# Kernel tuning notes

Measured on AMD Instinct MI355X. Metric: run time of the kernel, lower is better.

The kernel has to match this reference:

```python
import jax, jax.numpy as jnp
import numpy as np

S, B, F, H, L = 256, 64, 512, 512, 4
INV_SQRT_H = float(1.0 / np.sqrt(H))


def _ln(x, g, b, eps=1e-5):
    # torch nn.LayerNorm: biased variance, eps=1e-5
    mu = jnp.mean(x, axis=-1, keepdims=True)
    var = jnp.var(x, axis=-1, keepdims=True)
    return (x - mu) * jax.lax.rsqrt(var + eps) * g + b


def setup_inputs() -> dict:
    key = jax.random.key(0)
    k1, k2 = jax.random.split(key)
    x = jax.random.normal(k1, (S, B, F), dtype=jnp.float32)  # time-major [S,B,F]
    W = jax.random.normal(k2, (L, 6, F, H), dtype=jnp.float32) * 0.02  # q,k,v,i,f,o
    b = jnp.zeros((L, 6, H), jnp.float32)
    ln_g = jnp.ones((L, 6, H), jnp.float32)
    ln_b = jnp.zeros((L, 6, H), jnp.float32)
    return {"x": x, "W": W, "b": b, "ln_g": ln_g, "ln_b": ln_b}


def reference(x, W, b, ln_g, ln_b):
    # Dropout is identity (eval mode / p effectively 0).
    def step(carry, x_t):
        h, c, n = carry  # each [L,B,H]
        layer_input = x_t  # [B,F]
        hs, cs, ns = [], [], []
        for l in range(L):
            # all 6 gate projections in one einsum: [6,B,H]
            z = jnp.einsum('bf,gfh->gbh', layer_input, W[l]) + b[l][:, None, :]
            z = z.at[1].multiply(INV_SQRT_H)  # k = Wk(x)/sqrt(H) before LN
            z = _ln(z, ln_g[l][:, None, :], ln_b[l][:, None, :])
            q, k, v = z[0], z[1], z[2]
            i = jax.nn.sigmoid(z[3])
            f = jax.nn.sigmoid(z[4])
            o = jax.nn.sigmoid(z[5])
            # (k[:,:,None] @ v[:,None,:]).sum(dim=1) == k.sum(-1,keepdims)*v
            kv_sum = jnp.sum(k, axis=-1, keepdims=True) * v
            c_l = f * c[l] + i * kv_sum
            n_l = f * n[l] + i * k
            n_hat = n_l / (jnp.linalg.norm(n_l, axis=-1, keepdims=True) + 1e-8)
            h_l = o * jnp.tanh(q * n_hat)
            if l > 0:  # residual_conn
                h_l = h_l + layer_input
            layer_input = h_l
            hs.append(h_l); cs.append(c_l); ns.append(n_l)
        h = jnp.stack(hs); c = jnp.stack(cs); n = jnp.stack(ns)
        return (h, c, n), h[-1]

    init = tuple(jnp.zeros((L, B, H), x.dtype) for _ in range(3))
    (h, c, n), out = jax.lax.scan(step, init, x)  # out: [S,B,H] time-major
    return out, h, c, n
```

## Files before the change

kernel.cpp:

```cpp
#include <hip/hip_runtime.h>


typedef unsigned short u16;
typedef unsigned int   u32;
typedef short s8v  __attribute__((ext_vector_type(8)));
typedef float f16v __attribute__((ext_vector_type(16)));

#define S_    256
#define B_    64
#define F_    512
#define H_    512
#define L_    4
#define NG    3072
#define RALL  16384
#define CH    16
#define INV_SQRT_H 0.044194173824159216f

__device__ __forceinline__ float bu2f(u16 u) {
    union { u32 i; float f; } z; z.i = ((u32)u) << 16; return z.f;
}
__device__ __forceinline__ u16 f2bf(float f) {
    union { float f; u32 i; } z; z.f = f;
    u32 r = (z.i + 0x7FFFu + ((z.i >> 16) & 1u)) >> 16;
    return (u16)r;
}
__device__ __forceinline__ float sigm(float x)  { return 1.0f / (1.0f + __expf(-x)); }
__device__ __forceinline__ float tanhf_(float x){ return 2.0f / (1.0f + __expf(-2.0f * x)) - 1.0f; }
__device__ __forceinline__ float wred64(float v) {
    #pragma unroll
    for (int m = 1; m < 64; m <<= 1) v += __shfl_xor(v, m);
    return v;
}
__device__ __forceinline__ void gl_lds16(const u16* g, u16* l) {
    __builtin_amdgcn_global_load_lds((const __attribute__((address_space(1))) u32*)g,
                                     (__attribute__((address_space(3))) u32*)l, 16, 0, 0);
}
__device__ __forceinline__ void unp8(uint4 u, float* f) {
    f[0] = bu2f((u16)(u.x & 0xffff)); f[1] = bu2f((u16)(u.x >> 16));
    f[2] = bu2f((u16)(u.y & 0xffff)); f[3] = bu2f((u16)(u.y >> 16));
    f[4] = bu2f((u16)(u.z & 0xffff)); f[5] = bu2f((u16)(u.z >> 16));
    f[6] = bu2f((u16)(u.w & 0xffff)); f[7] = bu2f((u16)(u.w >> 16));
}
__device__ __forceinline__ uint4 pck8(const float* f) {
    uint4 u;
    u.x = (u32)f2bf(f[0]) | ((u32)f2bf(f[1]) << 16);
    u.y = (u32)f2bf(f[2]) | ((u32)f2bf(f[3]) << 16);
    u.z = (u32)f2bf(f[4]) | ((u32)f2bf(f[5]) << 16);
    u.w = (u32)f2bf(f[6]) | ((u32)f2bf(f[7]) << 16);
    return u;
}

__global__ void convw_k(const float* __restrict__ W, u16* __restrict__ WT) {
    __shared__ float tile[32][33];
    const int lg = blockIdx.z;
    const int h0 = blockIdx.x * 32, f0 = blockIdx.y * 32;
    const float* Wb = W  + (size_t)lg * F_ * H_;
    u16*        WTb = WT + (size_t)lg * F_ * H_;
    const int tx = threadIdx.x, ty = threadIdx.y;
    #pragma unroll
    for (int i = 0; i < 32; i += 8)
        tile[ty + i][tx] = Wb[(size_t)(f0 + ty + i) * H_ + h0 + tx];
    __syncthreads();
    #pragma unroll
    for (int i = 0; i < 32; i += 8)
        WTb[(size_t)(h0 + ty + i) * F_ + f0 + tx] = f2bf(tile[tx][ty + i]);
}

__global__ void convx_k(const float* __restrict__ x, u16* __restrict__ A) {
    const int i = blockIdx.x * 256 + threadIdx.x;
    float4 v = ((const float4*)x)[i];
    u32 lo = (u32)f2bf(v.x) | ((u32)f2bf(v.y) << 16);
    u32 hi = (u32)f2bf(v.z) | ((u32)f2bf(v.w) << 16);
    ((uint2*)A)[i] = make_uint2(lo, hi);
}

__global__ __launch_bounds__(256) void gemm_k(const u16* __restrict__ A,
                                              const u16* __restrict__ BT,
                                              u16* __restrict__ Z,
                                              const float* __restrict__ bias,
                                              int arow0) {
    __shared__ u16 lsA[128 * 64];
    __shared__ u16 lsB[128 * 64];
    const int t = threadIdx.x;
    const int ntile = blockIdx.x;
    const int mtile = blockIdx.y;
    const int ncol0 = ntile * 128;
    const u16* Ab = A  + (size_t)(arow0 + mtile * 128) * F_;
    const u16* Bb = BT + (size_t)ntile * 128 * F_;
    const int lane = t & 63, wv = t >> 6;

    f16v acc[2][2];
    #pragma unroll
    for (int i = 0; i < 2; i++)
        #pragma unroll
        for (int j = 0; j < 2; j++) acc[i][j] = 0.0f;

    const int wm = (wv >> 1) * 64, wn = (wv & 1) * 64;
    const int rl = lane & 31, hi = lane >> 5;
    const int r7 = rl & 7;

    int goff[4];
    #pragma unroll
    for (int s = 0; s < 4; s++) {
        const int c = t + 256 * s;
        const int row = c >> 3, slot = c & 7;
        const int g = slot ^ (row & 7);
        goff[s] = row * F_ + g * 8;
    }

    for (int kb = 0; kb < 8; ++kb) {
        const int kofs = kb * 64;
        #pragma unroll
        for (int s = 0; s < 4; s++) {
            const int c = t + 256 * s;
            gl_lds16(Ab + goff[s] + kofs, lsA + c * 8);
            gl_lds16(Bb + goff[s] + kofs, lsB + c * 8);
        }
        __syncthreads();
        #pragma unroll
        for (int s = 0; s < 4; ++s) {
            const int slot = ((s << 1) + hi) ^ r7;
            s8v fa[2], fb[2];
            #pragma unroll
            for (int i = 0; i < 2; i++)
                fa[i] = *(const s8v*)(lsA + (wm + i * 32 + rl) * 64 + slot * 8);
            #pragma unroll
            for (int j = 0; j < 2; j++)
                fb[j] = *(const s8v*)(lsB + (wn + j * 32 + rl) * 64 + slot * 8);
            #pragma unroll
            for (int i = 0; i < 2; i++)
                #pragma unroll
                for (int j = 0; j < 2; j++)
                    acc[i][j] = __builtin_amdgcn_mfma_f32_32x32x16_bf16(fa[i], fb[j], acc[i][j], 0, 0, 0);
        }
        __syncthreads();
    }

    #pragma unroll
    for (int j = 0; j < 2; j++) {
        const int col = ncol0 + wn + j * 32 + rl;
        const float bv = bias[col];
        #pragma unroll
        for (int i = 0; i < 2; i++) {
            const int mbase = mtile * 128 + wm + i * 32 + hi * 4;
            #pragma unroll
            for (int reg = 0; reg < 16; reg++) {
                const int row = mbase + (reg & 3) + 8 * (reg >> 2);
                Z[(size_t)row * NG + col] = f2bf(acc[i][j][reg] + bv);
            }
        }
    }
}

__global__ __launch_bounds__(256) void stats_k(const u16* __restrict__ Z,
                                               const float* __restrict__ lng1,
                                               const float* __restrict__ lnb1,
                                               float* __restrict__ stats) {
    const int wid = threadIdx.x >> 6, lane = threadIdx.x & 63;
    const int row = blockIdx.x * 4 + wid;
    const u16* zr = Z + (size_t)row * NG + lane * 8;

    float g1v[8], b1v[8];
    #pragma unroll
    for (int j = 0; j < 8; j++) { g1v[j] = lng1[lane * 8 + j]; b1v[j] = lnb1[lane * 8 + j]; }

    float s[4], sq[4], wk = 0.f, sg1 = 0.f, sb1 = 0.f;
    #pragma unroll
    for (int g = 0; g < 4; ++g) {
        uint4 u = *(const uint4*)(zr + (g + 1) * 512);
        float f[8];
        unp8(u, f);
        float ls = 0.f, lq = 0.f;
        #pragma unroll
        for (int j = 0; j < 8; j++) { ls += f[j]; lq += f[j] * f[j]; }
        s[g] = ls; sq[g] = lq;
        if (g == 0) {
            #pragma unroll
            for (int j = 0; j < 8; j++) wk += g1v[j] * f[j];
        }
    }
    #pragma unroll
    for (int j = 0; j < 8; j++) { sg1 += g1v[j]; sb1 += b1v[j]; }

    #pragma unroll
    for (int g = 0; g < 4; ++g) { s[g] = wred64(s[g]); sq[g] = wred64(sq[g]); }
    wk = wred64(wk); sg1 = wred64(sg1); sb1 = wred64(sb1);

    if (lane == 0) {
        float* o = stats + (size_t)row * 16;
        const float inv = 1.0f / 512.0f;
        float mu1 = 0.f, rs1 = 0.f;
        #pragma unroll
        for (int g = 0; g < 4; ++g) {
            float m = s[g] * inv, e2 = sq[g] * inv;
            if (g == 0) { m *= INV_SQRT_H; e2 *= INV_SQRT_H * INV_SQRT_H; }
            const float rs = rsqrtf(fmaxf(e2 - m * m, 0.0f) + 1e-5f);
            o[1 + g] = m; o[7 + g] = rs;
            if (g == 0) { mu1 = m; rs1 = rs; }
        }
        o[12] = rs1 * (INV_SQRT_H * wk - mu1 * sg1) + sb1;
    }
}

__global__ __launch_bounds__(128) void scanA_k(const u16* __restrict__ Z,
                                               const float* __restrict__ stats,
                                               const float* __restrict__ lngl,
                                               const float* __restrict__ lnbl,
                                               u16* __restrict__ nbuf,
                                               u16* __restrict__ pbuf,
                                               float* __restrict__ sumP,
                                               float* __restrict__ sumC,
                                               float* __restrict__ sumN) {
    const int b = blockIdx.y, chunk = blockIdx.z;
    const int h = blockIdx.x * 128 + threadIdx.x;
    __shared__ float sst[CH][16];
    for (int i = threadIdx.x; i < CH * 16; i += 128) {
        const int tc = i >> 4, j = i & 15;
        sst[tc][j] = stats[(size_t)((chunk * CH + tc) * 64 + b) * 16 + j];
    }
    float gg[4], gb[4];
    #pragma unroll
    for (int g = 0; g < 4; ++g) {
        gg[g] = lngl[(g + 1) * 512 + h];
        gb[g] = lnbl[(g + 1) * 512 + h];
    }
    __syncthreads();

    float c = 0.f, n = 0.f, P = 1.f;
    #pragma unroll 4
    for (int tc = 0; tc < CH; ++tc) {
        const int r = (chunk * CH + tc) * 64 + b;
        const u16* zr = Z + (size_t)r * NG + h;
        const float z1 = bu2f(zr[512]);
        const float z2 = bu2f(zr[1024]);
        const float z3 = bu2f(zr[1536]);
        const float z4 = bu2f(zr[2048]);
        const float kk = (z1 * INV_SQRT_H - sst[tc][1]) * sst[tc][7] * gg[0] + gb[0];
        const float vv = (z2 - sst[tc][2]) * sst[tc][8]  * gg[1] + gb[1];
        const float ii = sigm((z3 - sst[tc][3]) * sst[tc][9]  * gg[2] + gb[2]);
        const float ff = sigm((z4 - sst[tc][4]) * sst[tc][10] * gg[3] + gb[3]);
        c = ff * c + ii * (sst[tc][12] * vv);
        n = ff * n + ii * kk;
        P *= ff;
        nbuf[(size_t)r * 512 + h] = f2bf(n);
        pbuf[(size_t)r * 512 + h] = f2bf(P);
    }
    const size_t idx = ((size_t)chunk << 15) + (b << 9) + h;
    sumP[idx] = P; sumC[idx] = c; sumN[idx] = n;
}

__global__ __launch_bounds__(256) void scanB_k(const float* __restrict__ sumP,
                                               const float* __restrict__ sumC,
                                               const float* __restrict__ sumN,
                                               float* __restrict__ n0buf,
                                               float* __restrict__ cstate,
                                               float* __restrict__ nstate,
                                               float* __restrict__ finals,
                                               int t0, int NC, int l) {
    const int idx = blockIdx.x * 256 + threadIdx.x;
    float c, n;
    if (t0 == 0) { c = 0.f; n = 0.f; }
    else { c = cstate[idx]; n = nstate[idx]; }
    for (int ch = 0; ch < NC; ++ch) {
        const size_t o = ((size_t)ch << 15) + idx;
        n0buf[o] = n;
        const float P = sumP[o];
        c = sumC[o] + P * c;
        n = sumN[o] + P * n;
    }
    if (t0 + NC * CH == S_) {
        const int b = idx >> 9, h = idx & 511;
        const size_t so = ((size_t)l * B_ + b) * H_ + h;
        finals[(size_t)L_ * B_ * H_ + so] = c;
        finals[(size_t)2 * L_ * B_ * H_ + so] = n;
    } else {
        cstate[idx] = c; nstate[idx] = n;
    }
}

__global__ __launch_bounds__(256) void normh_k(const u16* __restrict__ Z,
                                               const u16* __restrict__ nbuf,
                                               const u16* __restrict__ pbuf,
                                               const float* __restrict__ n0buf,
                                               const float* __restrict__ lngl,
                                               const float* __restrict__ lnbl,
                                               float* __restrict__ hbuf,
                                               u16* __restrict__ aoutB,
                                               float* __restrict__ outp,
                                               float* __restrict__ finals,
                                               int t0, int l) {
    const int wid = threadIdx.x >> 6, lane = threadIdx.x & 63;
    const int r = blockIdx.x * 4 + wid;
    const int h0 = lane * 8;

    float nl[8], pv[8];
    unp8(*(const uint4*)(nbuf + (size_t)r * 512 + h0), nl);
    unp8(*(const uint4*)(pbuf + (size_t)r * 512 + h0), pv);
    const float* n0r = n0buf + ((size_t)(r >> 10) << 15) + ((size_t)(r & 63) << 9) + h0;
    const float4 na = *(const float4*)(n0r);
    const float4 nb = *(const float4*)(n0r + 4);
    const float n0v[8] = {na.x, na.y, na.z, na.w, nb.x, nb.y, nb.z, nb.w};

    const u16* zr = Z + (size_t)r * NG;
    float z0[8], z5[8];
    unp8(*(const uint4*)(zr + h0), z0);
    unp8(*(const uint4*)(zr + 2560 + h0), z5);

    float nsq = 0.f, s0 = 0.f, q0 = 0.f, s5 = 0.f, q5 = 0.f;
    float nv[8];
    #pragma unroll
    for (int j = 0; j < 8; j++) {
        nv[j] = fmaf(pv[j], n0v[j], nl[j]);
        nsq += nv[j] * nv[j];
        s0 += z0[j]; q0 += z0[j] * z0[j];
        s5 += z5[j]; q5 += z5[j] * z5[j];
    }
    nsq = wred64(nsq);
    s0 = wred64(s0); q0 = wred64(q0);
    s5 = wred64(s5); q5 = wred64(q5);
    const float rinv = 1.0f / (sqrtf(nsq) + 1e-8f);
    const float inv = 1.0f / 512.0f;
    const float mu0 = s0 * inv, mu5 = s5 * inv;
    const float rs0 = rsqrtf(fmaxf(q0 * inv - mu0 * mu0, 0.0f) + 1e-5f);
    const float rs5 = rsqrtf(fmaxf(q5 * inv - mu5 * mu5, 0.0f) + 1e-5f);

    float g0[8], b0[8], g5[8], b5[8];
    #pragma unroll
    for (int j = 0; j < 8; j++) {
        g0[j] = lngl[h0 + j];        b0[j] = lnbl[h0 + j];
        g5[j] = lngl[2560 + h0 + j]; b5[j] = lnbl[2560 + h0 + j];
    }

    const int tl = r >> 6, b = r & 63;
    const int gr = t0 + tl;
    const size_t grow = (((size_t)gr * 64 + b) * 512) + h0;

    float hv[8];
    #pragma unroll
    for (int j = 0; j < 8; j++) {
        const float q  = (z0[j] - mu0) * rs0 * g0[j] + b0[j];
        const float oo = sigm((z5[j] - mu5) * rs5 * g5[j] + b5[j]);
        hv[j] = oo * tanhf_(q * nv[j] * rinv);
    }
    if (l > 0) {
        #pragma unroll
        for (int j = 0; j < 8; j++) hv[j] += hbuf[grow + j];
    }
    if (outp) {
        #pragma unroll
        for (int j = 0; j < 8; j++) outp[grow + j] = hv[j];
    } else {
        #pragma unroll
        for (int j = 0; j < 8; j++) hbuf[grow + j] = hv[j];
    }
    if (aoutB) *(uint4*)(aoutB + grow) = pck8(hv);

    if (gr == S_ - 1) {
        const size_t so = (((size_t)l * B_ + b) * 512) + h0;
        #pragma unroll
        for (int j = 0; j < 8; j++) finals[so + j] = hv[j];
    }
}

extern "C" void kernel_launch(void* const* d_in, const int* in_sizes, int n_in,
                              void* d_out, int out_size, void* d_ws, size_t ws_size,
                              hipStream_t stream) {
    const float* x   = (const float*)d_in[0];
    const float* W   = (const float*)d_in[1];
    const float* bia = (const float*)d_in[2];
    const float* lng = (const float*)d_in[3];
    const float* lnb = (const float*)d_in[4];
    float* out = (float*)d_out;

    const size_t WT_B = (size_t)L_ * 6 * H_ * F_ * 2;
    const size_t A_B  = (size_t)RALL * F_ * 2;
    const size_t ST_B = (size_t)RALL * 16 * 4;
    const size_t CS_B = (size_t)B_ * H_ * 4;
    const size_t HB_B = (size_t)RALL * H_ * 4;
    auto zB  = [](int T) { return (size_t)T * B_ * NG * 2; };
    auto nB  = [](int T) { return (size_t)T * B_ * H_ * 2; };
    auto cxB = [](int T) { return (size_t)(T / CH) * B_ * H_ * 4; };
    const size_t base = WT_B + A_B + ST_B + 2 * CS_B + HB_B + 32768;

    int T = 16;
    const int cand[3] = {256, 64, 16};
    for (int i = 0; i < 3; i++) {
        const int Tc = cand[i];
        if (ws_size >= base + zB(Tc) + 2 * nB(Tc) + 4 * cxB(Tc)) { T = Tc; break; }
    }
    const int NC = T / CH;

    char* ws = (char*)d_ws;
    size_t off = 0;
    auto take = [&](size_t nb) { size_t o = off; off += (nb + 255) & ~(size_t)255; return o; };
    u16*   WT    = (u16*)  (ws + take(WT_B));
    u16*   Abf   = (u16*)  (ws + take(A_B));
    float* stats = (float*)(ws + take(ST_B));
    float* cs    = (float*)(ws + take(CS_B));
    float* ns    = (float*)(ws + take(CS_B));
    float* hbuf  = (float*)(ws + take(HB_B));
    u16*   zb    = (u16*)  (ws + take(zB(T)));
    u16*   nbuf  = (u16*)  (ws + take(nB(T)));
    u16*   pbuf  = (u16*)  (ws + take(nB(T)));
    float* sumP  = (float*)(ws + take(cxB(T)));
    float* sumC  = (float*)(ws + take(cxB(T)));
    float* sumN  = (float*)(ws + take(cxB(T)));
    float* n0buf = (float*)(ws + take(cxB(T)));

    convw_k<<<dim3(16, 16, 24), dim3(32, 8), 0, stream>>>(W, WT);
    convx_k<<<dim3(RALL * F_ / 4 / 256), dim3(256), 0, stream>>>(x, Abf);

    float* finals = out + (size_t)S_ * B_ * H_;
    for (int l = 0; l < L_; ++l) {
        const u16*   WTl   = WT  + (size_t)l * 6 * H_ * F_;
        const float* biasl = bia + (size_t)l * NG;
        const float* lngl  = lng + (size_t)l * 6 * H_;
        const float* lnbl  = lnb + (size_t)l * 6 * H_;
        for (int j = 0; j < S_ / T; ++j) {
            const int t0 = j * T, arow0 = t0 * B_;
            const int rows = T * B_;
            gemm_k<<<dim3(24, rows / 128), dim3(256), 0, stream>>>(Abf, WTl, zb, biasl, arow0);
            stats_k<<<dim3(rows / 4), dim3(256), 0, stream>>>(zb, lngl + H_, lnbl + H_, stats);
            scanA_k<<<dim3(4, B_, NC), dim3(128), 0, stream>>>(zb, stats, lngl, lnbl,
                                                               nbuf, pbuf, sumP, sumC, sumN);
            scanB_k<<<dim3(128), dim3(256), 0, stream>>>(sumP, sumC, sumN, n0buf,
                                                         cs, ns, finals, t0, NC, l);
            normh_k<<<dim3(rows / 4), dim3(256), 0, stream>>>(zb, nbuf, pbuf, n0buf,
                                                              lngl, lnbl, hbuf,
                                                              (l < 3) ? Abf : (u16*)nullptr,
                                                              (l == 3) ? out : (float*)nullptr,
                                                              finals, t0, l);
        }
    }
}
```

Baseline: 632.6 us.

## Fuse LN stats into scan kernel, drop fp32 residual buffer, relayout GEMM LDS

Merges the separate LayerNorm statistics kernel into the chunked scan kernel: each 512-thread block computes per-timestep row stats into shared memory before scanning, removing a launch and a global stats round trip. The per-layer gamma/beta sums are precomputed once. The fp32 residual buffer hbuf is removed, and the residual is read from the bf16 activation buffer, which lowers precision of the residual add. The GEMM's LDS staging is reorganised into an MFMA-fragment-ordered layout instead of an XOR-swizzled one.

```diff
diff --git a/kernel.cpp b/kernel.cpp
--- a/kernel.cpp
+++ b/kernel.cpp
@@ -31,6 +31,11 @@
     for (int m = 1; m < 64; m <<= 1) v += __shfl_xor(v, m);
     return v;
 }
+__device__ __forceinline__ float wred32(float v) {
+    #pragma unroll
+    for (int m = 1; m < 32; m <<= 1) v += __shfl_xor(v, m);
+    return v;
+}
 __device__ __forceinline__ void gl_lds16(const u16* g, u16* l) {
     __builtin_amdgcn_global_load_lds((const __attribute__((address_space(1))) u32*)g,
                                      (__attribute__((address_space(3))) u32*)l, 16, 0, 0);
@@ -74,13 +79,26 @@
     ((uint2*)A)[i] = make_uint2(lo, hi);
 }
 
+__global__ void sumgb_k(const float* __restrict__ lng, const float* __restrict__ lnb,
+                        float* __restrict__ sgb) {
+    const int l = blockIdx.x, lane = threadIdx.x;
+    float s = 0.f, b = 0.f;
+    #pragma unroll
+    for (int j = 0; j < 8; j++) {
+        s += lng[(size_t)l * 6 * 512 + 512 + j * 64 + lane];
+        b += lnb[(size_t)l * 6 * 512 + 512 + j * 64 + lane];
+    }
+    s = wred64(s); b = wred64(b);
+    if (lane == 0) { sgb[l * 2] = s; sgb[l * 2 + 1] = b; }
+}
+
 __global__ __launch_bounds__(256) void gemm_k(const u16* __restrict__ A,
                                               const u16* __restrict__ BT,
                                               u16* __restrict__ Z,
                                               const float* __restrict__ bias,
                                               int arow0) {
-    __shared__ u16 lsA[128 * 64];
-    __shared__ u16 lsB[128 * 64];
+    __shared__ u16 lsA[8192];
+    __shared__ u16 lsB[8192];
     const int t = threadIdx.x;
     const int ntile = blockIdx.x;
     const int mtile = blockIdx.y;
@@ -88,6 +106,8 @@
     const u16* Ab = A  + (size_t)(arow0 + mtile * 128) * F_;
     const u16* Bb = BT + (size_t)ntile * 128 * F_;
     const int lane = t & 63, wv = t >> 6;
+    const int rl = lane & 31, hi = lane >> 5;
+    const int wm = (wv >> 1) * 64, wn = (wv & 1) * 64;
 
     f16v acc[2][2];
     #pragma unroll
@@ -95,38 +115,33 @@
         #pragma unroll
         for (int j = 0; j < 2; j++) acc[i][j] = 0.0f;
 
-    const int wm = (wv >> 1) * 64, wn = (wv & 1) * 64;
-    const int rl = lane & 31, hi = lane >> 5;
-    const int r7 = rl & 7;
-
     int goff[4];
     #pragma unroll
-    for (int s = 0; s < 4; s++) {
-        const int c = t + 256 * s;
-        const int row = c >> 3, slot = c & 7;
-        const int g = slot ^ (row & 7);
-        goff[s] = row * F_ + g * 8;
+    for (int jj = 0; jj < 4; jj++) {
+        const int idx = wv * 4 + jj;
+        const int p = idx >> 3, s = (idx >> 1) & 3, i = idx & 1;
+        goff[jj] = (p * 64 + i * 32 + rl) * F_ + s * 16 + hi * 8;
     }
 
     for (int kb = 0; kb < 8; ++kb) {
         const int kofs = kb * 64;
         #pragma unroll
-        for (int s = 0; s < 4; s++) {
-            const int c = t + 256 * s;
-            gl_lds16(Ab + goff[s] + kofs, lsA + c * 8);
-            gl_lds16(Bb + goff[s] + kofs, lsB + c * 8);
+        for (int jj = 0; jj < 4; jj++) {
+            u16* dst = (u16*)((char*)nullptr) ;
+            const int dof = ((wv * 4 + jj) * 64 + lane) * 8;
+            gl_lds16(Ab + goff[jj] + kofs, lsA + dof);
+            gl_lds16(Bb + goff[jj] + kofs, lsB + dof);
         }
         __syncthreads();
         #pragma unroll
         for (int s = 0; s < 4; ++s) {
-            const int slot = ((s << 1) + hi) ^ r7;
+            const int pa = ((wv >> 1) * 8 + s * 2) * 512 + lane * 8;
+            const int pb = ((wv & 1) * 8 + s * 2) * 512 + lane * 8;
             s8v fa[2], fb[2];
             #pragma unroll
-            for (int i = 0; i < 2; i++)
-                fa[i] = *(const s8v*)(lsA + (wm + i * 32 + rl) * 64 + slot * 8);
-            #pragma unroll
-            for (int j = 0; j < 2; j++)
-                fb[j] = *(const s8v*)(lsB + (wn + j * 32 + rl) * 64 + slot * 8);
+            for (int i = 0; i < 2; i++) fa[i] = *(const s8v*)(lsA + pa + i * 512);
+            #pragma unroll
+            for (int j = 0; j < 2; j++) fb[j] = *(const s8v*)(lsB + pb + j * 512);
             #pragma unroll
             for (int i = 0; i < 2; i++)
                 #pragma unroll
@@ -152,80 +167,71 @@
     }
 }
 
-__global__ __launch_bounds__(256) void stats_k(const u16* __restrict__ Z,
-                                               const float* __restrict__ lng1,
-                                               const float* __restrict__ lnb1,
-                                               float* __restrict__ stats) {
-    const int wid = threadIdx.x >> 6, lane = threadIdx.x & 63;
-    const int row = blockIdx.x * 4 + wid;
-    const u16* zr = Z + (size_t)row * NG + lane * 8;
-
-    float g1v[8], b1v[8];
-    #pragma unroll
-    for (int j = 0; j < 8; j++) { g1v[j] = lng1[lane * 8 + j]; b1v[j] = lnb1[lane * 8 + j]; }
-
-    float s[4], sq[4], wk = 0.f, sg1 = 0.f, sb1 = 0.f;
-    #pragma unroll
-    for (int g = 0; g < 4; ++g) {
-        uint4 u = *(const uint4*)(zr + (g + 1) * 512);
-        float f[8];
-        unp8(u, f);
-        float ls = 0.f, lq = 0.f;
-        #pragma unroll
-        for (int j = 0; j < 8; j++) { ls += f[j]; lq += f[j] * f[j]; }
-        s[g] = ls; sq[g] = lq;
-        if (g == 0) {
-            #pragma unroll
-            for (int j = 0; j < 8; j++) wk += g1v[j] * f[j];
-        }
-    }
-    #pragma unroll
-    for (int j = 0; j < 8; j++) { sg1 += g1v[j]; sb1 += b1v[j]; }
-
-    #pragma unroll
-    for (int g = 0; g < 4; ++g) { s[g] = wred64(s[g]); sq[g] = wred64(sq[g]); }
-    wk = wred64(wk); sg1 = wred64(sg1); sb1 = wred64(sb1);
-
-    if (lane == 0) {
-        float* o = stats + (size_t)row * 16;
-        const float inv = 1.0f / 512.0f;
-        float mu1 = 0.f, rs1 = 0.f;
-        #pragma unroll
-        for (int g = 0; g < 4; ++g) {
-            float m = s[g] * inv, e2 = sq[g] * inv;
-            if (g == 0) { m *= INV_SQRT_H; e2 *= INV_SQRT_H * INV_SQRT_H; }
-            const float rs = rsqrtf(fmaxf(e2 - m * m, 0.0f) + 1e-5f);
-            o[1 + g] = m; o[7 + g] = rs;
-            if (g == 0) { mu1 = m; rs1 = rs; }
-        }
-        o[12] = rs1 * (INV_SQRT_H * wk - mu1 * sg1) + sb1;
-    }
-}
-
-__global__ __launch_bounds__(128) void scanA_k(const u16* __restrict__ Z,
-                                               const float* __restrict__ stats,
+__global__ __launch_bounds__(512) void sscan_k(const u16* __restrict__ Z,
                                                const float* __restrict__ lngl,
                                                const float* __restrict__ lnbl,
+                                               const float* __restrict__ sgb,
                                                u16* __restrict__ nbuf,
                                                u16* __restrict__ pbuf,
                                                float* __restrict__ sumP,
                                                float* __restrict__ sumC,
                                                float* __restrict__ sumN) {
-    const int b = blockIdx.y, chunk = blockIdx.z;
-    const int h = blockIdx.x * 128 + threadIdx.x;
+    const int b = blockIdx.x, chunk = blockIdx.y;
+    const int t = threadIdx.x;
     __shared__ float sst[CH][16];
-    for (int i = threadIdx.x; i < CH * 16; i += 128) {
-        const int tc = i >> 4, j = i & 15;
-        sst[tc][j] = stats[(size_t)((chunk * CH + tc) * 64 + b) * 16 + j];
-    }
+
+    {
+        const int tc = t >> 5, l5 = t & 31;
+        const int r = (chunk * CH + tc) * 64 + b;
+        const u16* zr = Z + (size_t)r * NG + 512;
+        const float* g1 = lngl + 512;
+        float s[4], q[4], wk = 0.f;
+        #pragma unroll
+        for (int g = 0; g < 4; ++g) { s[g] = 0.f; q[g] = 0.f; }
+        #pragma unroll
+        for (int g = 0; g < 4; ++g) {
+            #pragma unroll
+            for (int half = 0; half < 2; ++half) {
+                const int col = half * 256 + l5 * 8;
+                uint4 u = *(const uint4*)(zr + g * 512 + col);
+                float f[8];
+                unp8(u, f);
+                #pragma unroll
+                for (int j = 0; j < 8; j++) { s[g] += f[j]; q[g] += f[j] * f[j]; }
+                if (g == 0) {
+                    const float4 ga = *(const float4*)(g1 + col);
+                    const float4 gb4 = *(const float4*)(g1 + col + 4);
+                    wk += ga.x * f[0] + ga.y * f[1] + ga.z * f[2] + ga.w * f[3]
+                        + gb4.x * f[4] + gb4.y * f[5] + gb4.z * f[6] + gb4.w * f[7];
+                }
+            }
+        }
+        #pragma unroll
+        for (int g = 0; g < 4; ++g) { s[g] = wred32(s[g]); q[g] = wred32(q[g]); }
+        wk = wred32(wk);
+        if (l5 == 0) {
+            const float inv = 1.0f / 512.0f;
+            float mu1 = 0.f, rs1 = 0.f;
+            #pragma unroll
+            for (int g = 0; g < 4; ++g) {
+                float m = s[g] * inv, e2 = q[g] * inv;
+                if (g == 0) { m *= INV_SQRT_H; e2 *= INV_SQRT_H * INV_SQRT_H; }
+                const float rs = rsqrtf(fmaxf(e2 - m * m, 0.0f) + 1e-5f);
+                sst[tc][1 + g] = m; sst[tc][7 + g] = rs;
+                if (g == 0) { mu1 = m; rs1 = rs; }
+            }
+            sst[tc][12] = rs1 * (INV_SQRT_H * wk - mu1 * sgb[0]) + sgb[1];
+        }
+    }
+    __syncthreads();
+
+    const int h = t;
     float gg[4], gb[4];
     #pragma unroll
     for (int g = 0; g < 4; ++g) {
         gg[g] = lngl[(g + 1) * 512 + h];
         gb[g] = lnbl[(g + 1) * 512 + h];
     }
-    __syncthreads();
-
     float c = 0.f, n = 0.f, P = 1.f;
     #pragma unroll 4
     for (int tc = 0; tc < CH; ++tc) {
@@ -284,8 +290,7 @@
                                                const float* __restrict__ n0buf,
                                                const float* __restrict__ lngl,
                                                const float* __restrict__ lnbl,
-                                               float* __restrict__ hbuf,
-                                               u16* __restrict__ aoutB,
+                                               u16* __restrict__ Abf,
                                                float* __restrict__ outp,
                                                float* __restrict__ finals,
                                                int t0, int l) {
@@ -343,17 +348,17 @@
         hv[j] = oo * tanhf_(q * nv[j] * rinv);
     }
     if (l > 0) {
-        #pragma unroll
-        for (int j = 0; j < 8; j++) hv[j] += hbuf[grow + j];
+        float rv[8];
+        unp8(*(const uint4*)(Abf + grow), rv);
+        #pragma unroll
+        for (int j = 0; j < 8; j++) hv[j] += rv[j];
     }
     if (outp) {
         #pragma unroll
         for (int j = 0; j < 8; j++) outp[grow + j] = hv[j];
     } else {
-        #pragma unroll
-        for (int j = 0; j < 8; j++) hbuf[grow + j] = hv[j];
-    }
-    if (aoutB) *(uint4*)(aoutB + grow) = pck8(hv);
+        *(uint4*)(Abf + grow) = pck8(hv);
+    }
 
     if (gr == S_ - 1) {
         const size_t so = (((size_t)l * B_ + b) * 512) + h0;
@@ -374,13 +379,11 @@
 
     const size_t WT_B = (size_t)L_ * 6 * H_ * F_ * 2;
     const size_t A_B  = (size_t)RALL * F_ * 2;
-    const size_t ST_B = (size_t)RALL * 16 * 4;
     const size_t CS_B = (size_t)B_ * H_ * 4;
-    const size_t HB_B = (size_t)RALL * H_ * 4;
     auto zB  = [](int T) { return (size_t)T * B_ * NG * 2; };
     auto nB  = [](int T) { return (size_t)T * B_ * H_ * 2; };
     auto cxB = [](int T) { return (size_t)(T / CH) * B_ * H_ * 4; };
-    const size_t base = WT_B + A_B + ST_B + 2 * CS_B + HB_B + 32768;
+    const size_t base = WT_B + A_B + 2 * CS_B + 65536;
 
     int T = 16;
     const int cand[3] = {256, 64, 16};
@@ -395,10 +398,9 @@
     auto take = [&](size_t nb) { size_t o = off; off += (nb + 255) & ~(size_t)255; return o; };
     u16*   WT    = (u16*)  (ws + take(WT_B));
     u16*   Abf   = (u16*)  (ws + take(A_B));
-    float* stats = (float*)(ws + take(ST_B));
+    float* sgb   = (float*)(ws + take(256));
     float* cs    = (float*)(ws + take(CS_B));
     float* ns    = (float*)(ws + take(CS_B));
-    float* hbuf  = (float*)(ws + take(HB_B));
     u16*   zb    = (u16*)  (ws + take(zB(T)));
     u16*   nbuf  = (u16*)  (ws + take(nB(T)));
     u16*   pbuf  = (u16*)  (ws + take(nB(T)));
@@ -409,6 +411,7 @@
 
     convw_k<<<dim3(16, 16, 24), dim3(32, 8), 0, stream>>>(W, WT);
     convx_k<<<dim3(RALL * F_ / 4 / 256), dim3(256), 0, stream>>>(x, Abf);
+    sumgb_k<<<dim3(L_), dim3(64), 0, stream>>>(lng, lnb, sgb);
 
     float* finals = out + (size_t)S_ * B_ * H_;
     for (int l = 0; l < L_; ++l) {
@@ -420,14 +423,12 @@
             const int t0 = j * T, arow0 = t0 * B_;
             const int rows = T * B_;
             gemm_k<<<dim3(24, rows / 128), dim3(256), 0, stream>>>(Abf, WTl, zb, biasl, arow0);
-            stats_k<<<dim3(rows / 4), dim3(256), 0, stream>>>(zb, lngl + H_, lnbl + H_, stats);
-            scanA_k<<<dim3(4, B_, NC), dim3(128), 0, stream>>>(zb, stats, lngl, lnbl,
-                                                               nbuf, pbuf, sumP, sumC, sumN);
+            sscan_k<<<dim3(B_, NC), dim3(512), 0, stream>>>(zb, lngl, lnbl, sgb + l * 2,
+                                                            nbuf, pbuf, sumP, sumC, sumN);
             scanB_k<<<dim3(128), dim3(256), 0, stream>>>(sumP, sumC, sumN, n0buf,
                                                          cs, ns, finals, t0, NC, l);
             normh_k<<<dim3(rows / 4), dim3(256), 0, stream>>>(zb, nbuf, pbuf, n0buf,
-                                                              lngl, lnbl, hbuf,
-                                                              (l < 3) ? Abf : (u16*)nullptr,
+                                                              lngl, lnbl, Abf,
                                                               (l == 3) ? out : (float*)nullptr,
                                                               finals, t0, l);
         }
```

After: 741.1 us. 1.17x slower.
